# Kernel tuning notes

Measured on AMD Instinct MI355X. Metric: run time of the kernel, lower is better.

Reference implementation:

```python
import jax, jax.numpy as jnp
import numpy as np

N = 16384          # nodes/edges
F = 128            # features per rank
L_MAX = 3
SIZES = [1, 3, 9, 27]   # 3^l components for l = 0..3

def _doublefactorial(n):
    x = 1
    for i in range(1, n + 1, 2):
        x *= i
    return x

def _factorial(n):
    x = 1
    for i in range(1, n + 1):
        x *= i
    return x

def _norm_l1l2l3(l1, l2, l3):
    # even-parity recoupling normalization (verbatim from source)
    J = l1 + l2 + l3
    J1 = J - 2 * l1 - 1
    J2 = J - 2 * l2 - 1
    J3 = J - 2 * l3 - 1
    num = (_factorial(l1) * _factorial(l2) * _doublefactorial(2 * l3 - 1)
           * _factorial((J1 + 1) // 2) * _factorial((J2 + 1) // 2))
    den = (_factorial(l3) * _doublefactorial(J1) * _doublefactorial(J2)
           * _doublefactorial(J3) * _factorial(J // 2))
    return num / den

# All even-parity recoupling paths (l1, l2, l3): triangle inequality + even l1+l2-l3.
PATHS = [(l1, l2, l3)
         for l3 in range(L_MAX + 1)
         for l1 in range(L_MAX + 1)
         for l2 in range(L_MAX + 1)
         if abs(l1 - l2) <= l3 <= l1 + l2 and (l1 + l2 - l3) % 2 == 0]
N_PATHS = len(PATHS)  # == 23 == _get_n_paths(3,3,3)

def setup_inputs() -> dict:
    key = jax.random.key(0)
    k1, k2, k3 = jax.random.split(key, 3)
    x = jax.random.normal(k1, (N, F * sum(SIZES)), dtype=jnp.float32)
    y = jax.random.normal(k2, (N, F * sum(SIZES)), dtype=jnp.float32)
    weights = jax.random.normal(k3, (N_PATHS, F), dtype=jnp.float32)
    return {"x": x, "y": y, "weights": weights}

def _split(t):
    # flat [N, F*40] -> list of [N, F, 3,...,3] (rank-l Cartesian blocks)
    blocks, off = [], 0
    for l, s in enumerate(SIZES):
        blocks.append(t[:, off:off + F * s].reshape((-1, F) + (3,) * l))
        off += F * s
    return blocks

def reference(x, y, weights):
    xs = _split(x)
    ys = _split(y)
    outs = [jnp.zeros((x.shape[0], F) + (3,) * l3, x.dtype) for l3 in range(L_MAX + 1)]
    for p, (l1, l2, l3) in enumerate(PATHS):
        k = (l1 + l2 - l3) // 2          # number of contracted Cartesian indices
        xa = 'abc'[:l1 - k]              # free indices from x
        c = 'uvw'[:k]                    # contracted indices
        yb = 'deg'[:l2 - k]              # free indices from y
        sub = f"nf{xa}{c},nf{c}{yb}->nf{xa}{yb}"
        z = jnp.einsum(sub, xs[l1], ys[l2])           # [N, F, 3^l3]
        w = weights[p].reshape((1, F) + (1,) * l3)    # per-path per-feature weight
        outs[l3] = outs[l3] + jnp.asarray(_norm_l1l2l3(l1, l2, l3), x.dtype) * w * z
    return jnp.concatenate([o.reshape(o.shape[0], -1) for o in outs], axis=1)
```

## Files before the change

### kernel.cpp

```cpp
#include <hip/hip_runtime.h>


#define FF 128
#define ROW 5120
#define HALFROW 2560

typedef float floatx4 __attribute__((ext_vector_type(4)));

__device__ __constant__ float NORMS[23] = {
    1.0f, 1.0f, 2.0f/3.0f, 0.4f,
    1.0f, 1.0f, 1.0f, 1.0f, 2.0f/3.0f, 2.0f/3.0f,
    1.0f, 0.75f, 1.0f, 1.0f, 1.0f, 1.0f, 0.75f,
    1.0f, 5.0f/9.0f, 5.0f/9.0f, 5.0f/6.0f, 1.0f, 5.0f/6.0f
};

#define GL2LDS(g, l)  __builtin_amdgcn_global_load_lds(                      \
        (const __attribute__((address_space(1))) void*)(g),                  \
        (__attribute__((address_space(3))) void*)(l), 16, 0, 0)

__device__ __forceinline__ int rowoff(int o, int fbase) {
    if (o < 64)  return fbase       + o;
    if (o < 256) return 128 + fbase*3  + (o-64);
    if (o < 832) return 512 + fbase*9  + (o-256);
    return 1664 + fbase*27 + (o-832);
}

__global__ __launch_bounds__(128) void wtp_kernel(
    const float* __restrict__ x, const float* __restrict__ y,
    const float* __restrict__ w, float* __restrict__ out)
{
    __shared__ float buf[2 * HALFROW];

    const int tid   = threadIdx.x;
    const int f     = tid & 63;
    const int half  = tid >> 6;
    const int wbase = half * 256;

    const int n     = blockIdx.x >> 1;
    const int fbase = (blockIdx.x & 1) << 6;

    const float* xr = x + (size_t)n * ROW;
    const float* yr = y + (size_t)n * ROW;
    float* orow     = out + (size_t)n * ROW;

    int goff[5];
    #pragma unroll
    for (int i = 0; i < 5; ++i) goff[i] = rowoff(i * 512 + tid * 4, fbase);

    #pragma unroll
    for (int i = 0; i < 5; ++i) {
        GL2LDS(xr + goff[i], buf + i * 512 + wbase);
        GL2LDS(yr + goff[i], buf + HALFROW + i * 512 + wbase);
    }

    float c[23];
    #pragma unroll
    for (int p = 0; p < 23; ++p) c[p] = NORMS[p] * w[p * FF + fbase + f];

    asm volatile("s_waitcnt vmcnt(0)" ::: "memory");
    __syncthreads();

    const float* bx = buf;
    const float* by = buf + HALFROW;
    const float x0 = bx[f], y0 = by[f];
    float x1[3], y1[3], x2[9], y2[9];
    #pragma unroll
    for (int j = 0; j < 3; ++j)  x1[j] = bx[64  + f*3 + j];
    #pragma unroll
    for (int j = 0; j < 3; ++j)  y1[j] = by[64  + f*3 + j];
    #pragma unroll
    for (int j = 0; j < 9; ++j)  x2[j] = bx[256 + f*9 + j];
    #pragma unroll
    for (int j = 0; j < 9; ++j)  y2[j] = by[256 + f*9 + j];

    const float* bx3 = bx + 832 + f*27;
    const float* by3 = by + 832 + f*27;

    float o0, o1[3], o2[9], o3[27];

    if (half == 0) {
        {
            float acc = c[0] * (x0 * y0);
            float d3 = 0.f;
            #pragma unroll
            for (int u = 0; u < 3; ++u) d3 += x1[u] * y1[u];
            acc += c[1] * d3;
            float d9 = 0.f;
            #pragma unroll
            for (int t = 0; t < 9; ++t) d9 += x2[t] * y2[t];
            acc += c[2] * d9;
            float d27 = 0.f;
            #pragma unroll
            for (int t = 0; t < 27; ++t) d27 += bx3[t] * by3[t];
            acc += c[3] * d27;
            o0 = acc;
        }
        #pragma unroll
        for (int d = 0; d < 3; ++d) {
            float acc = c[4] * (x0 * y1[d]) + c[5] * (x1[d] * y0);
            float s6 = 0.f, s7 = 0.f, s8 = 0.f, s9 = 0.f;
            #pragma unroll
            for (int u = 0; u < 3; ++u) s6 += x1[u] * y2[u*3 + d];
            #pragma unroll
            for (int u = 0; u < 3; ++u) s7 += x2[d*3 + u] * y1[u];
            #pragma unroll
            for (int t = 0; t < 9; ++t) s8 += x2[t] * by3[t*3 + d];
            #pragma unroll
            for (int t = 0; t < 9; ++t) s9 += bx3[d*9 + t] * y2[t];
            o1[d] = acc + c[6]*s6 + c[7]*s7 + c[8]*s8 + c[9]*s9;
        }
        #pragma unroll
        for (int t = 0; t < 9; ++t) {
            const int a = t / 3, d = t % 3;
            float acc = c[10] * (x0 * y2[t]) + c[11] * (x1[a] * y1[d])
                      + c[13] * (x2[t] * y0);
            float s12 = 0.f, s14 = 0.f, s15 = 0.f, s16 = 0.f;
            #pragma unroll
            for (int u = 0; u < 3; ++u) s12 += x1[u] * by3[u*9 + t];
            #pragma unroll
            for (int u = 0; u < 3; ++u) s14 += x2[a*3 + u] * y2[u*3 + d];
            #pragma unroll
            for (int u = 0; u < 3; ++u) s15 += bx3[t*3 + u] * y1[u];
            #pragma unroll
            for (int s = 0; s < 9; ++s) s16 += bx3[a*9 + s] * by3[s*3 + d];
            o2[t] = acc + c[12]*s12 + c[14]*s14 + c[15]*s15 + c[16]*s16;
        }
    } else {
        #pragma unroll
        for (int q = 0; q < 27; ++q) {
            const int a = q / 9, t9 = q % 9, r = q / 3, e = q % 3;
            float acc = c[17] * (x0 * by3[q]) + c[18] * (x1[a] * y2[t9])
                      + c[19] * (x2[r] * y1[e]) + c[21] * (bx3[q] * y0);
            float s20 = 0.f, s22 = 0.f;
            #pragma unroll
            for (int u = 0; u < 3; ++u) s20 += x2[a*3 + u] * by3[u*9 + t9];
            #pragma unroll
            for (int u = 0; u < 3; ++u) s22 += bx3[r*3 + u] * y2[u*3 + e];
            o3[q] = acc + c[20]*s20 + c[22]*s22;
        }
    }
    __syncthreads();

    if (half == 0) {
        buf[f] = o0;
        #pragma unroll
        for (int d = 0; d < 3; ++d) buf[64  + f*3 + d] = o1[d];
        #pragma unroll
        for (int t = 0; t < 9; ++t) buf[256 + f*9 + t] = o2[t];
    } else {
        #pragma unroll
        for (int q = 0; q < 27; ++q) buf[832 + f*27 + q] = o3[q];
    }
    __syncthreads();

    #pragma unroll
    for (int i = 0; i < 5; ++i) {
        floatx4 v = *(const floatx4*)(buf + i * 512 + tid * 4);
        __builtin_nontemporal_store(v, (floatx4*)(orow + goff[i]));
    }
}

extern "C" void kernel_launch(void* const* d_in, const int* in_sizes, int n_in,
                              void* d_out, int out_size, void* d_ws, size_t ws_size,
                              hipStream_t stream) {
    const float* x = (const float*)d_in[0];
    const float* y = (const float*)d_in[1];
    const float* w = (const float*)d_in[2];
    float* out = (float*)d_out;

    const int n_nodes = in_sizes[0] / ROW;
    dim3 grid(n_nodes * 2), block(128);
    hipLaunchKernelGGL(wtp_kernel, grid, block, 0, stream, x, y, w, out);
}
```

Measured before the change: 178.0 us.

## Persistent blocks with double-buffered LDS prefetch of next node

```diff
diff --git a/kernel.cpp b/kernel.cpp
--- a/kernel.cpp
+++ b/kernel.cpp
@@ -18,145 +18,177 @@
         (const __attribute__((address_space(1))) void*)(g),                  \
         (__attribute__((address_space(3))) void*)(l), 16, 0, 0)
 
-__device__ __forceinline__ int rowoff(int o, int fbase) {
-    if (o < 64)  return fbase       + o;
-    if (o < 256) return 128 + fbase*3  + (o-64);
-    if (o < 832) return 512 + fbase*9  + (o-256);
-    return 1664 + fbase*27 + (o-832);
-}
-
-__global__ __launch_bounds__(128) void wtp_kernel(
+__global__ __launch_bounds__(128, 2) void wtp_kernel(
     const float* __restrict__ x, const float* __restrict__ y,
-    const float* __restrict__ w, float* __restrict__ out)
+    const float* __restrict__ w, float* __restrict__ out, int n_nodes)
 {
-    __shared__ float buf[2 * HALFROW];
+    __shared__ float buf[2][2 * HALFROW];
 
     const int tid   = threadIdx.x;
     const int f     = tid & 63;
     const int half  = tid >> 6;
     const int wbase = half * 256;
 
-    const int n     = blockIdx.x >> 1;
-    const int fbase = (blockIdx.x & 1) << 6;
-
-    const float* xr = x + (size_t)n * ROW;
-    const float* yr = y + (size_t)n * ROW;
-    float* orow     = out + (size_t)n * ROW;
+    const int bslot = blockIdx.x & 511;
+    const int fbase = (blockIdx.x >> 9) << 6;
+    const int chunk = n_nodes >> 9;
+    const int first = bslot * chunk;
 
     int goff[5];
     #pragma unroll
-    for (int i = 0; i < 5; ++i) goff[i] = rowoff(i * 512 + tid * 4, fbase);
-
-    #pragma unroll
     for (int i = 0; i < 5; ++i) {
-        GL2LDS(xr + goff[i], buf + i * 512 + wbase);
-        GL2LDS(yr + goff[i], buf + HALFROW + i * 512 + wbase);
+        const int o = i * 512 + tid * 4;
+        int r;
+        if      (o < 64)  r = fbase        + o;
+        else if (o < 256) r = 128 + fbase*3  + (o - 64);
+        else if (o < 832) r = 512 + fbase*9  + (o - 256);
+        else              r = 1664 + fbase*27 + (o - 832);
+        goff[i] = r;
+    }
+
+    {
+        const float* xr = x + (size_t)first * ROW;
+        const float* yr = y + (size_t)first * ROW;
+        #pragma unroll
+        for (int i = 0; i < 5; ++i) {
+            GL2LDS(xr + goff[i], &buf[0][i * 512 + wbase]);
+            GL2LDS(yr + goff[i], &buf[0][HALFROW + i * 512 + wbase]);
+        }
     }
 
     float c[23];
     #pragma unroll
     for (int p = 0; p < 23; ++p) c[p] = NORMS[p] * w[p * FF + fbase + f];
 
-    asm volatile("s_waitcnt vmcnt(0)" ::: "memory");
-    __syncthreads();
-
-    const float* bx = buf;
-    const float* by = buf + HALFROW;
-    const float x0 = bx[f], y0 = by[f];
-    float x1[3], y1[3], x2[9], y2[9];
-    #pragma unroll
-    for (int j = 0; j < 3; ++j)  x1[j] = bx[64  + f*3 + j];
-    #pragma unroll
-    for (int j = 0; j < 3; ++j)  y1[j] = by[64  + f*3 + j];
-    #pragma unroll
-    for (int j = 0; j < 9; ++j)  x2[j] = bx[256 + f*9 + j];
-    #pragma unroll
-    for (int j = 0; j < 9; ++j)  y2[j] = by[256 + f*9 + j];
-
-    const float* bx3 = bx + 832 + f*27;
-    const float* by3 = by + 832 + f*27;
-
-    float o0, o1[3], o2[9], o3[27];
-
-    if (half == 0) {
-        {
-            float acc = c[0] * (x0 * y0);
-            float d3 = 0.f;
-            #pragma unroll
-            for (int u = 0; u < 3; ++u) d3 += x1[u] * y1[u];
-            acc += c[1] * d3;
-            float d9 = 0.f;
-            #pragma unroll
-            for (int t = 0; t < 9; ++t) d9 += x2[t] * y2[t];
-            acc += c[2] * d9;
-            float d27 = 0.f;
-            #pragma unroll
-            for (int t = 0; t < 27; ++t) d27 += bx3[t] * by3[t];
-            acc += c[3] * d27;
-            o0 = acc;
-        }
-        #pragma unroll
-        for (int d = 0; d < 3; ++d) {
-            float acc = c[4] * (x0 * y1[d]) + c[5] * (x1[d] * y0);
-            float s6 = 0.f, s7 = 0.f, s8 = 0.f, s9 = 0.f;
-            #pragma unroll
-            for (int u = 0; u < 3; ++u) s6 += x1[u] * y2[u*3 + d];
-            #pragma unroll
-            for (int u = 0; u < 3; ++u) s7 += x2[d*3 + u] * y1[u];
-            #pragma unroll
-            for (int t = 0; t < 9; ++t) s8 += x2[t] * by3[t*3 + d];
-            #pragma unroll
-            for (int t = 0; t < 9; ++t) s9 += bx3[d*9 + t] * y2[t];
-            o1[d] = acc + c[6]*s6 + c[7]*s7 + c[8]*s8 + c[9]*s9;
-        }
-        #pragma unroll
-        for (int t = 0; t < 9; ++t) {
-            const int a = t / 3, d = t % 3;
-            float acc = c[10] * (x0 * y2[t]) + c[11] * (x1[a] * y1[d])
-                      + c[13] * (x2[t] * y0);
-            float s12 = 0.f, s14 = 0.f, s15 = 0.f, s16 = 0.f;
-            #pragma unroll
-            for (int u = 0; u < 3; ++u) s12 += x1[u] * by3[u*9 + t];
-            #pragma unroll
-            for (int u = 0; u < 3; ++u) s14 += x2[a*3 + u] * y2[u*3 + d];
-            #pragma unroll
-            for (int u = 0; u < 3; ++u) s15 += bx3[t*3 + u] * y1[u];
-            #pragma unroll
-            for (int s = 0; s < 9; ++s) s16 += bx3[a*9 + s] * by3[s*3 + d];
-            o2[t] = acc + c[12]*s12 + c[14]*s14 + c[15]*s15 + c[16]*s16;
-        }
-    } else {
-        #pragma unroll
-        for (int q = 0; q < 27; ++q) {
-            const int a = q / 9, t9 = q % 9, r = q / 3, e = q % 3;
-            float acc = c[17] * (x0 * by3[q]) + c[18] * (x1[a] * y2[t9])
-                      + c[19] * (x2[r] * y1[e]) + c[21] * (bx3[q] * y0);
-            float s20 = 0.f, s22 = 0.f;
-            #pragma unroll
-            for (int u = 0; u < 3; ++u) s20 += x2[a*3 + u] * by3[u*9 + t9];
-            #pragma unroll
-            for (int u = 0; u < 3; ++u) s22 += bx3[r*3 + u] * y2[u*3 + e];
-            o3[q] = acc + c[20]*s20 + c[22]*s22;
-        }
-    }
-    __syncthreads();
-
-    if (half == 0) {
-        buf[f] = o0;
-        #pragma unroll
-        for (int d = 0; d < 3; ++d) buf[64  + f*3 + d] = o1[d];
-        #pragma unroll
-        for (int t = 0; t < 9; ++t) buf[256 + f*9 + t] = o2[t];
-    } else {
-        #pragma unroll
-        for (int q = 0; q < 27; ++q) buf[832 + f*27 + q] = o3[q];
-    }
-    __syncthreads();
-
-    #pragma unroll
-    for (int i = 0; i < 5; ++i) {
-        floatx4 v = *(const floatx4*)(buf + i * 512 + tid * 4);
-        __builtin_nontemporal_store(v, (floatx4*)(orow + goff[i]));
+    int cur = 0;
+    for (int k = 0; k < chunk; ++k) {
+        const int node = first + k;
+
+        if (k + 1 < chunk) {
+            const float* xr = x + (size_t)(node + 1) * ROW;
+            const float* yr = y + (size_t)(node + 1) * ROW;
+            float* nb = &buf[cur ^ 1][0];
+            #pragma unroll
+            for (int i = 0; i < 5; ++i) {
+                GL2LDS(xr + goff[i], nb + i * 512 + wbase);
+                GL2LDS(yr + goff[i], nb + HALFROW + i * 512 + wbase);
+            }
+            if (k == 0) {
+                asm volatile("s_waitcnt vmcnt(10)" ::: "memory");
+            } else {
+                asm volatile("s_waitcnt vmcnt(15)" ::: "memory");
+            }
+        } else {
+            asm volatile("s_waitcnt vmcnt(0)" ::: "memory");
+        }
+        __builtin_amdgcn_s_barrier();
+
+        const float* bx = &buf[cur][0];
+        const float* by = &buf[cur][HALFROW];
+        const float x0 = bx[f], y0 = by[f];
+        float x1[3], y1[3], x2[9], y2[9];
+        #pragma unroll
+        for (int j = 0; j < 3; ++j)  x1[j] = bx[64  + f*3 + j];
+        #pragma unroll
+        for (int j = 0; j < 3; ++j)  y1[j] = by[64  + f*3 + j];
+        #pragma unroll
+        for (int j = 0; j < 9; ++j)  x2[j] = bx[256 + f*9 + j];
+        #pragma unroll
+        for (int j = 0; j < 9; ++j)  y2[j] = by[256 + f*9 + j];
+
+        const float* bx3 = bx + 832 + f*27;
+        const float* by3 = by + 832 + f*27;
+
+        float o0, o1[3], o2[9], o3[27];
+
+        if (half == 0) {
+            {
+                float acc = c[0] * (x0 * y0);
+                float d3 = 0.f;
+                #pragma unroll
+                for (int u = 0; u < 3; ++u) d3 += x1[u] * y1[u];
+                acc += c[1] * d3;
+                float d9 = 0.f;
+                #pragma unroll
+                for (int t = 0; t < 9; ++t) d9 += x2[t] * y2[t];
+                acc += c[2] * d9;
+                float d27 = 0.f;
+                #pragma unroll
+                for (int t = 0; t < 27; ++t) d27 += bx3[t] * by3[t];
+                acc += c[3] * d27;
+                o0 = acc;
+            }
+            #pragma unroll
+            for (int d = 0; d < 3; ++d) {
+                float acc = c[4] * (x0 * y1[d]) + c[5] * (x1[d] * y0);
+                float s6 = 0.f, s7 = 0.f, s8 = 0.f, s9 = 0.f;
+                #pragma unroll
+                for (int u = 0; u < 3; ++u) s6 += x1[u] * y2[u*3 + d];
+                #pragma unroll
+                for (int u = 0; u < 3; ++u) s7 += x2[d*3 + u] * y1[u];
+                #pragma unroll
+                for (int t = 0; t < 9; ++t) s8 += x2[t] * by3[t*3 + d];
+                #pragma unroll
+                for (int t = 0; t < 9; ++t) s9 += bx3[d*9 + t] * y2[t];
+                o1[d] = acc + c[6]*s6 + c[7]*s7 + c[8]*s8 + c[9]*s9;
+            }
+            #pragma unroll
+            for (int t = 0; t < 9; ++t) {
+                const int a = t / 3, d = t % 3;
+                float acc = c[10] * (x0 * y2[t]) + c[11] * (x1[a] * y1[d])
+                          + c[13] * (x2[t] * y0);
+                float s12 = 0.f, s14 = 0.f, s15 = 0.f, s16 = 0.f;
+                #pragma unroll
+                for (int u = 0; u < 3; ++u) s12 += x1[u] * by3[u*9 + t];
+                #pragma unroll
+                for (int u = 0; u < 3; ++u) s14 += x2[a*3 + u] * y2[u*3 + d];
+                #pragma unroll
+                for (int u = 0; u < 3; ++u) s15 += bx3[t*3 + u] * y1[u];
+                #pragma unroll
+                for (int s = 0; s < 9; ++s) s16 += bx3[a*9 + s] * by3[s*3 + d];
+                o2[t] = acc + c[12]*s12 + c[14]*s14 + c[15]*s15 + c[16]*s16;
+            }
+        } else {
+            #pragma unroll
+            for (int q = 0; q < 27; ++q) {
+                const int a = q / 9, t9 = q % 9, r = q / 3, e = q % 3;
+                float acc = c[17] * (x0 * by3[q]) + c[18] * (x1[a] * y2[t9])
+                          + c[19] * (x2[r] * y1[e]) + c[21] * (bx3[q] * y0);
+                float s20 = 0.f, s22 = 0.f;
+                #pragma unroll
+                for (int u = 0; u < 3; ++u) s20 += x2[a*3 + u] * by3[u*9 + t9];
+                #pragma unroll
+                for (int u = 0; u < 3; ++u) s22 += bx3[r*3 + u] * y2[u*3 + e];
+                o3[q] = acc + c[20]*s20 + c[22]*s22;
+            }
+        }
+
+        asm volatile("s_waitcnt lgkmcnt(0)" ::: "memory");
+        __builtin_amdgcn_s_barrier();
+
+        float* B = &buf[cur][0];
+        if (half == 0) {
+            B[f] = o0;
+            #pragma unroll
+            for (int d = 0; d < 3; ++d) B[64  + f*3 + d] = o1[d];
+            #pragma unroll
+            for (int t = 0; t < 9; ++t) B[256 + f*9 + t] = o2[t];
+        } else {
+            #pragma unroll
+            for (int q = 0; q < 27; ++q) B[832 + f*27 + q] = o3[q];
+        }
+        asm volatile("s_waitcnt lgkmcnt(0)" ::: "memory");
+        __builtin_amdgcn_s_barrier();
+
+        float* orow = out + (size_t)node * ROW;
+        #pragma unroll
+        for (int i = 0; i < 5; ++i) {
+            floatx4 v = *(const floatx4*)(B + i * 512 + tid * 4);
+            __builtin_nontemporal_store(v, (floatx4*)(orow + goff[i]));
+        }
+        asm volatile("s_waitcnt lgkmcnt(0)" ::: "memory");
+        __builtin_amdgcn_s_barrier();
+        cur ^= 1;
     }
 }
 
@@ -169,6 +201,6 @@
     float* out = (float*)d_out;
 
     const int n_nodes = in_sizes[0] / ROW;
-    dim3 grid(n_nodes * 2), block(128);
-    hipLaunchKernelGGL(wtp_kernel, grid, block, 0, stream, x, y, w, out);
+    dim3 grid(1024), block(128);
+    hipLaunchKernelGGL(wtp_kernel, grid, block, 0, stream, x, y, w, out, n_nodes);
 }
```

Measured after the change: 217.7 us. +22.3%, slower.
